# Kernel optimization log

Hardware: AMD Instinct MI355X
Metric: run time of the kernel (lower is better)

## Reference

```python
import jax, jax.numpy as jnp
import numpy as np

FILTER_SIZE = 27           # filter_size (K + 2)
K = FILTER_SIZE - 2        # sampled neighbors per central node
FEAT = 512                 # feature_dim
HID = 512                  # hidden_dim
NUM_NODES = 100000         # node-id universe for the features() embedding
B = 20000                  # batch of central nodes
ALPHA = 0.2                # leaky relu slope


def _star_eigvec(fs):
    # eigenvectors of I - D A D for the star graph on `fs` nodes (node 0 = hub)
    A = np.zeros((fs, fs))
    A[0, 1:] = 1.0
    A[1:, 0] = 1.0
    D = np.eye(fs)
    D[0, 0] = (fs - 1) ** (-0.5)
    L = np.eye(fs) - D @ A @ D
    _, u = np.linalg.eigh(L)
    return u.astype(np.float32)


def setup_inputs() -> dict:
    key = jax.random.key(0)
    k1, k2, k3, k4, k5 = jax.random.split(key, 5)
    nodes = jax.random.randint(k1, (B,), 0, NUM_NODES)
    neigh = jax.random.randint(k2, (B, K), 0, NUM_NODES)
    feat_table = jax.random.normal(k3, (NUM_NODES, FEAT), dtype=jnp.float32)
    # xavier_uniform for W [FEAT, HID] and a [2*HID]
    limW = float(np.sqrt(6.0 / (FEAT + HID)))
    W = jax.random.uniform(k4, (FEAT, HID), minval=-limW, maxval=limW, dtype=jnp.float32)
    lima = float(np.sqrt(6.0 / (1 + 2 * HID)))
    a_vec = jax.random.uniform(k5, (2 * HID,), minval=-lima, maxval=lima, dtype=jnp.float32)
    U = jnp.asarray(_star_eigvec(FILTER_SIZE))
    return {"nodes": nodes, "neigh": neigh, "feat_table": feat_table,
            "W": W, "a_vec": a_vec, "U": U}


def reference(nodes, neigh, feat_table, W, a_vec, U):
    # project features: input2 (central), input1 (neighbors)
    h_ct = feat_table[nodes] @ W                              # [B, H]
    h_nb = jnp.einsum('bkf,fh->bkh', feat_table[neigh], W)    # [B, K, H]
    # GAT-style edge scores: a @ [h_ct ; h_nb]
    s_ct = h_ct @ a_vec[:HID]                                 # [B]
    s_nb = h_nb @ a_vec[HID:]                                 # [B, K]
    logits = s_ct[:, None] + s_nb                             # [B, K]
    lrelu = jnp.where(logits > 0, logits, ALPHA * logits)
    edge_e = jnp.exp(-lrelu)                                  # [B, K]
    # per-row normalization (equals dense a1 rowsum: neighbors per row distinct)
    attn = edge_e / jnp.sum(edge_e, axis=1, keepdims=True)    # [B, K]
    # mask1: slots 1..K of each filter_size block hold attn * h_nb
    mask = attn[..., None] * h_nb                             # [B, K, H]
    m = jnp.pad(mask, ((0, 0), (1, 1), (0, 0)))               # [B, FILTER_SIZE, H]
    mt = jnp.swapaxes(m, 1, 2)                                # [B, H, FILTER_SIZE]
    # spectral transform: (mt @ U @ U^T) @ ones[FILTER_SIZE,1]
    avg = jnp.ones((FILTER_SIZE, 1), dtype=m.dtype)
    temp = ((mt @ U) @ U.T) @ avg                             # [B, H, 1]
    out = jnp.squeeze(temp, axis=-1)                          # [B, H]
    return jax.nn.relu(out)
```

## Files before the change

kernel.cpp:

```cpp
#include <hip/hip_runtime.h>
#include <stdint.h>
#include <string.h>

#define FEAT 512
#define HID 512
#define KNB 25
#define FS 27
#define NNODES 100000
#define ALPHA 0.2f

typedef short bf16x8 __attribute__((ext_vector_type(8)));
typedef float f32x4 __attribute__((ext_vector_type(4)));

__device__ __forceinline__ float bf2f(unsigned short u) {
    union { unsigned int i; float f; } x; x.i = ((unsigned int)u) << 16; return x.f;
}
__device__ __forceinline__ unsigned short f2bf(float f) {
    unsigned int x = __float_as_uint(f);
    unsigned int r = (x + 0x7fffu + ((x >> 16) & 1u)) >> 16;
    return (unsigned short)r;
}
__device__ __forceinline__ float ldf(const void* base, size_t idx, bool isf32) {
    return isf32 ? ((const float*)base)[idx] : bf2f(((const unsigned short*)base)[idx]);
}
__device__ __forceinline__ void gload16(const void* g, void* lds) {
    __builtin_amdgcn_global_load_lds(
        (const __attribute__((address_space(1))) unsigned int*)g,
        (__attribute__((address_space(3))) unsigned int*)lds, 16, 0, 0);
}

__global__ void detect_dtype(const void* __restrict__ feat, int* __restrict__ flag) {
    __shared__ int cnt;
    if (threadIdx.x == 0) cnt = 0;
    __syncthreads();
    const unsigned short* u = (const unsigned short*)feat;
    int c = 0;
    for (int i = threadIdx.x; i < 2048; i += 256) {
        float av = fabsf(bf2f(u[i]));
        if (!(av < 1e4f)) c++;
    }
    atomicAdd(&cnt, c);
    __syncthreads();
    if (threadIdx.x == 0) *flag = (cnt > 16) ? 1 : 0;
}

__global__ void prep_pq(const void* __restrict__ W, const void* __restrict__ a_vec,
                        const int* __restrict__ flag,
                        float* __restrict__ p, float* __restrict__ q) {
    bool isf32 = (*flag != 0);
    int f = blockIdx.x;
    int lane = threadIdx.x;
    float accp = 0.f, accq = 0.f;
    #pragma unroll
    for (int j = 0; j < 8; ++j) {
        int h = lane * 8 + j;
        float wv = ldf(W, (size_t)f * HID + h, isf32);
        accq += wv * ldf(a_vec, h, isf32);
        accp += wv * ldf(a_vec, HID + h, isf32);
    }
    #pragma unroll
    for (int off = 32; off > 0; off >>= 1) {
        accp += __shfl_down(accp, off);
        accq += __shfl_down(accq, off);
    }
    if (lane == 0) { p[f] = accp; q[f] = accq; }
}

__global__ void prep_M(const void* __restrict__ U, const int* __restrict__ flag,
                       float* __restrict__ Mv) {
    __shared__ float cs[FS];
    bool isf32 = (*flag != 0);
    int t = threadIdx.x;
    if (t < FS) {
        float c = 0.f;
        for (int i = 0; i < FS; ++i) c += ldf(U, i * FS + t, isf32);
        cs[t] = c;
    }
    __syncthreads();
    if (t < FS) {
        float m = 0.f;
        for (int j = 0; j < FS; ++j) m += ldf(U, t * FS + j, isf32) * cs[j];
        Mv[t] = m;
    }
}

__global__ void transposeW(const void* __restrict__ W, const int* __restrict__ flag,
                           unsigned short* __restrict__ Wt) {
    bool isf32 = (*flag != 0);
    int idx = blockIdx.x * blockDim.x + threadIdx.x;
    int n = idx >> 9, k = idx & (HID - 1);
    Wt[idx] = f2bf(ldf(W, (size_t)k * HID + n, isf32));
}

__global__ __launch_bounds__(256) void convert_score(
    const void* __restrict__ feat, const float* __restrict__ p,
    const float* __restrict__ q, const int* __restrict__ flag,
    unsigned short* __restrict__ featbf, float* __restrict__ sp,
    float* __restrict__ sq, int nRows) {
    bool isf32 = (*flag != 0);
    int wave = threadIdx.x >> 6, lane = threadIdx.x & 63;
    int row = blockIdx.x * 4 + wave;
    if (row >= nRows) return;
    float vals[8];
    if (isf32) {
        const float4* src = (const float4*)((const float*)feat + (size_t)row * FEAT) + lane * 2;
        float4 v0 = src[0], v1 = src[1];
        vals[0] = v0.x; vals[1] = v0.y; vals[2] = v0.z; vals[3] = v0.w;
        vals[4] = v1.x; vals[5] = v1.y; vals[6] = v1.z; vals[7] = v1.w;
        unsigned short o[8];
        #pragma unroll
        for (int j = 0; j < 8; ++j) o[j] = f2bf(vals[j]);
        *(uint4*)(&featbf[(size_t)row * FEAT + lane * 8]) = *(const uint4*)o;
    } else {
        uint4 v = *((const uint4*)((const unsigned short*)feat + (size_t)row * FEAT) + lane);
        unsigned int w4[4] = {v.x, v.y, v.z, v.w};
        #pragma unroll
        for (int j = 0; j < 4; ++j) {
            vals[2 * j]     = __uint_as_float(w4[j] << 16);
            vals[2 * j + 1] = __uint_as_float(w4[j] & 0xffff0000u);
        }
    }
    float accp = 0.f, accq = 0.f;
    const float* pv = p + lane * 8;
    const float* qv = q + lane * 8;
    #pragma unroll
    for (int j = 0; j < 8; ++j) { accp += vals[j] * pv[j]; accq += vals[j] * qv[j]; }
    #pragma unroll
    for (int off = 32; off > 0; off >>= 1) {
        accp += __shfl_down(accp, off);
        accq += __shfl_down(accq, off);
    }
    if (lane == 0) { sp[row] = accp; sq[row] = accq; }
}

__global__ __launch_bounds__(256) void attn_gather2(
    const void* __restrict__ feat, const unsigned short* __restrict__ featbf,
    const int* __restrict__ nodes, const int* __restrict__ neigh,
    const float* __restrict__ sp, const float* __restrict__ sq,
    const float* __restrict__ Mv, const int* __restrict__ flag,
    unsigned short* __restrict__ g, int B) {
    bool isf32 = (*flag != 0);
    const unsigned short* F = isf32 ? featbf : (const unsigned short*)feat;
    int wave = threadIdx.x >> 6, lane = threadIdx.x & 63;
    int b = blockIdx.x * 4 + wave;
    if (b >= B) return;
    int id = 0; float e = 0.f;
    if (lane < KNB) {
        id = neigh[(size_t)b * KNB + lane];
        float l = sq[nodes[b]] + sp[id];
        float lr = l > 0.f ? l : ALPHA * l;
        e = __expf(-lr);
    }
    float Z = e;
    #pragma unroll
    for (int off = 16; off > 0; off >>= 1) Z += __shfl_down(Z, off);
    Z = __shfl(Z, 0);
    float w = (lane < KNB) ? e * (1.f / Z) * Mv[lane + 1] : 0.f;
    float acc[8] = {0.f, 0.f, 0.f, 0.f, 0.f, 0.f, 0.f, 0.f};
    #pragma unroll
    for (int k = 0; k < KNB; ++k) {
        int idk = __builtin_amdgcn_readlane(id, k);
        float wk = __uint_as_float((unsigned int)__builtin_amdgcn_readlane(__float_as_int(w), k));
        uint4 v = *((const uint4*)(F + (size_t)idk * FEAT) + lane);
        unsigned int w4[4] = {v.x, v.y, v.z, v.w};
        #pragma unroll
        for (int j = 0; j < 4; ++j) {
            acc[2 * j]     += wk * __uint_as_float(w4[j] << 16);
            acc[2 * j + 1] += wk * __uint_as_float(w4[j] & 0xffff0000u);
        }
    }
    unsigned short o[8];
    #pragma unroll
    for (int j = 0; j < 8; ++j) o[j] = f2bf(acc[j]);
    *(uint4*)(&g[(size_t)b * FEAT + lane * 8]) = *(const uint4*)o;
}

__global__ __launch_bounds__(256) void attn_gather(
    const void* __restrict__ feat, const int* __restrict__ nodes,
    const int* __restrict__ neigh, const float* __restrict__ p,
    const float* __restrict__ q, const float* __restrict__ Mv,
    const int* __restrict__ flag, unsigned short* __restrict__ g) {
    __shared__ __attribute__((aligned(16))) unsigned short ldsF[KNB * FEAT];
    __shared__ float ldsS[KNB + 1];
    bool isf32 = (*flag != 0);
    int b = blockIdx.x;
    int t = threadIdx.x;
    int wave = t >> 6, lane = t & 63;
    for (int r = wave; r < KNB + 1; r += 4) {
        int id = (r == 0) ? nodes[b] : neigh[(size_t)b * KNB + (r - 1)];
        float vals[8];
        if (isf32) {
            const float4* row = (const float4*)((const float*)feat + (size_t)id * FEAT) + lane * 2;
            float4 v0 = row[0], v1 = row[1];
            vals[0] = v0.x; vals[1] = v0.y; vals[2] = v0.z; vals[3] = v0.w;
            vals[4] = v1.x; vals[5] = v1.y; vals[6] = v1.z; vals[7] = v1.w;
        } else {
            uint4 v = *((const uint4*)((const unsigned short*)feat + (size_t)id * FEAT) + lane);
            unsigned int w4[4] = {v.x, v.y, v.z, v.w};
            #pragma unroll
            for (int j = 0; j < 4; ++j) {
                vals[2 * j]     = bf2f((unsigned short)(w4[j] & 0xffffu));
                vals[2 * j + 1] = bf2f((unsigned short)(w4[j] >> 16));
            }
        }
        if (r > 0) {
            unsigned short o[8];
            #pragma unroll
            for (int j = 0; j < 8; ++j) o[j] = f2bf(vals[j]);
            *(uint4*)(&ldsF[(r - 1) * FEAT + lane * 8]) = *(const uint4*)o;
        }
        const float* vec = ((r == 0) ? q : p) + lane * 8;
        float acc = 0.f;
        #pragma unroll
        for (int j = 0; j < 8; ++j) acc += vals[j] * vec[j];
        #pragma unroll
        for (int off = 32; off > 0; off >>= 1) acc += __shfl_down(acc, off);
        if (lane == 0) ldsS[r] = acc;
    }
    __syncthreads();
    float s0 = ldsS[0];
    float w[KNB];
    float Z = 0.f;
    #pragma unroll
    for (int k = 0; k < KNB; ++k) {
        float l = s0 + ldsS[k + 1];
        float lr = l > 0.f ? l : ALPHA * l;
        float e = __expf(-lr);
        w[k] = e;
        Z += e;
    }
    float inv = 1.f / Z;
    #pragma unroll
    for (int k = 0; k < KNB; ++k) w[k] *= inv * Mv[k + 1];
    float acc0 = 0.f, acc1 = 0.f;
    #pragma unroll
    for (int k = 0; k < KNB; ++k) {
        unsigned int v = *(const unsigned int*)(&ldsF[k * FEAT + 2 * t]);
        acc0 += w[k] * bf2f((unsigned short)(v & 0xffffu));
        acc1 += w[k] * bf2f((unsigned short)(v >> 16));
    }
    unsigned int o = ((unsigned int)f2bf(acc1) << 16) | (unsigned int)f2bf(acc0);
    *(unsigned int*)(&g[(size_t)b * FEAT + 2 * t]) = o;
}

__global__ __launch_bounds__(256) void gemm_relu128(
    const unsigned short* __restrict__ G, const unsigned short* __restrict__ Wt,
    const int* __restrict__ flag, void* __restrict__ out, int M) {
    __shared__ __attribute__((aligned(16))) unsigned short As[128 * 64];
    __shared__ __attribute__((aligned(16))) unsigned short Bs[128 * 64];
    bool isf32 = (*flag != 0);
    int t = threadIdx.x;
    int wave = t >> 6, lane = t & 63;
    int mBase = blockIdx.y * 128;
    int nBase = blockIdx.x * 128;
    int wr = wave >> 1, wc = wave & 1;
    int fr = lane & 15, quad = lane >> 4;
    f32x4 acc[4][4];
    #pragma unroll
    for (int m = 0; m < 4; ++m)
        #pragma unroll
        for (int n = 0; n < 4; ++n) acc[m][n] = (f32x4){0.f, 0.f, 0.f, 0.f};

    int lrow = lane >> 3;
    int lcol = (lane & 7) * 8;
    for (int k0 = 0; k0 < FEAT; k0 += 64) {
        #pragma unroll
        for (int i = 0; i < 4; ++i) {
            int r = wave * 32 + i * 8;
            gload16(G + (size_t)(mBase + r + lrow) * FEAT + k0 + lcol, &As[r * 64]);
            gload16(Wt + (size_t)(nBase + r + lrow) * FEAT + k0 + lcol, &Bs[r * 64]);
        }
        __syncthreads();
        #pragma unroll
        for (int kk = 0; kk < 64; kk += 32) {
            bf16x8 av[4], bv[4];
            #pragma unroll
            for (int m = 0; m < 4; ++m)
                av[m] = *(const bf16x8*)(&As[(wr * 64 + m * 16 + fr) * 64 + kk + quad * 8]);
            #pragma unroll
            for (int n = 0; n < 4; ++n)
                bv[n] = *(const bf16x8*)(&Bs[(wc * 64 + n * 16 + fr) * 64 + kk + quad * 8]);
            #pragma unroll
            for (int m = 0; m < 4; ++m)
                #pragma unroll
                for (int n = 0; n < 4; ++n)
                    acc[m][n] = __builtin_amdgcn_mfma_f32_16x16x32_bf16(av[m], bv[n], acc[m][n], 0, 0, 0);
        }
        __syncthreads();
    }
    int col = lane & 15, qr = (lane >> 4) * 4;
    #pragma unroll
    for (int m = 0; m < 4; ++m) {
        #pragma unroll
        for (int n = 0; n < 4; ++n) {
            #pragma unroll
            for (int i = 0; i < 4; ++i) {
                int row = mBase + wr * 64 + m * 16 + qr + i;
                if (row < M) {
                    int cn = nBase + wc * 64 + n * 16 + col;
                    float v = acc[m][n][i];
                    v = v > 0.f ? v : 0.f;
                    size_t off = (size_t)row * HID + cn;
                    if (isf32) ((float*)out)[off] = v;
                    else ((unsigned short*)out)[off] = f2bf(v);
                }
            }
        }
    }
}

__global__ __launch_bounds__(256) void gemm_relu(
    const unsigned short* __restrict__ G, const unsigned short* __restrict__ Wt,
    const int* __restrict__ flag, void* __restrict__ out, int M) {
    __shared__ __attribute__((aligned(16))) unsigned short As[64 * 72];
    __shared__ __attribute__((aligned(16))) unsigned short Bs[64 * 72];
    bool isf32 = (*flag != 0);
    int t = threadIdx.x;
    int mBase = blockIdx.y * 64;
    int nBase = blockIdx.x * 64;
    int wave = t >> 6, lane = t & 63;
    int mOff = (wave & 1) * 32, nOff = (wave >> 1) * 32;
    f32x4 acc00 = {0.f, 0.f, 0.f, 0.f}, acc01 = {0.f, 0.f, 0.f, 0.f};
    f32x4 acc10 = {0.f, 0.f, 0.f, 0.f}, acc11 = {0.f, 0.f, 0.f, 0.f};
    int lr = t >> 2;
    int seg = (t & 3) * 16;
    int fr = lane & 15, quad = lane >> 4;
    for (int k0 = 0; k0 < FEAT; k0 += 64) {
        uint4 av0 = {0u, 0u, 0u, 0u}, av1 = {0u, 0u, 0u, 0u};
        int gr = mBase + lr;
        if (gr < M) {
            const unsigned short* s = G + (size_t)gr * FEAT + k0 + seg;
            av0 = *(const uint4*)s;
            av1 = *(const uint4*)(s + 8);
        }
        *(uint4*)(&As[lr * 72 + seg]) = av0;
        *(uint4*)(&As[lr * 72 + seg + 8]) = av1;
        const unsigned short* bs = Wt + (size_t)(nBase + lr) * FEAT + k0 + seg;
        *(uint4*)(&Bs[lr * 72 + seg]) = *(const uint4*)bs;
        *(uint4*)(&Bs[lr * 72 + seg + 8]) = *(const uint4*)(bs + 8);
        __syncthreads();
        #pragma unroll
        for (int kk = 0; kk < 64; kk += 32) {
            bf16x8 a0 = *(const bf16x8*)(&As[(mOff + fr) * 72 + kk + quad * 8]);
            bf16x8 a1 = *(const bf16x8*)(&As[(mOff + 16 + fr) * 72 + kk + quad * 8]);
            bf16x8 b0 = *(const bf16x8*)(&Bs[(nOff + fr) * 72 + kk + quad * 8]);
            bf16x8 b1 = *(const bf16x8*)(&Bs[(nOff + 16 + fr) * 72 + kk + quad * 8]);
            acc00 = __builtin_amdgcn_mfma_f32_16x16x32_bf16(a0, b0, acc00, 0, 0, 0);
            acc01 = __builtin_amdgcn_mfma_f32_16x16x32_bf16(a0, b1, acc01, 0, 0, 0);
            acc10 = __builtin_amdgcn_mfma_f32_16x16x32_bf16(a1, b0, acc10, 0, 0, 0);
            acc11 = __builtin_amdgcn_mfma_f32_16x16x32_bf16(a1, b1, acc11, 0, 0, 0);
        }
        __syncthreads();
    }
    int col = lane & 15, qr = (lane >> 4) * 4;
    #pragma unroll
    for (int sel = 0; sel < 4; ++sel) {
        f32x4 a = (sel == 0) ? acc00 : (sel == 1) ? acc01 : (sel == 2) ? acc10 : acc11;
        int mt = sel >> 1, nt = sel & 1;
        #pragma unroll
        for (int i = 0; i < 4; ++i) {
            int row = mBase + mOff + mt * 16 + qr + i;
            if (row < M) {
                int cn = nBase + nOff + nt * 16 + col;
                float v = a[i];
                v = v > 0.f ? v : 0.f;
                size_t off = (size_t)row * HID + cn;
                if (isf32) ((float*)out)[off] = v;
                else ((unsigned short*)out)[off] = f2bf(v);
            }
        }
    }
}

extern "C" void kernel_launch(void* const* d_in, const int* in_sizes, int n_in,
                              void* d_out, int out_size, void* d_ws, size_t ws_size,
                              hipStream_t stream) {
    const int* nodes = (const int*)d_in[0];
    const int* neigh = (const int*)d_in[1];
    const void* feat = d_in[2];
    const void* W = d_in[3];
    const void* a_vec = d_in[4];
    const void* U = d_in[5];
    int B = in_sizes[0];

    char* ws = (char*)d_ws;
    int* flag = (int*)ws;
    float* p = (float*)(ws + 256);
    float* q = (float*)(ws + 256 + 2048);
    float* Mv = (float*)(ws + 256 + 4096);
    unsigned short* Wt = (unsigned short*)(ws + 4608);
    unsigned short* g = (unsigned short*)(ws + 4608 + (size_t)FEAT * HID * 2);
    size_t gEnd = 4608 + (size_t)FEAT * HID * 2 + (size_t)B * FEAT * 2;
    float* sp = (float*)(ws + gEnd);
    float* sq = (float*)(ws + gEnd + (size_t)NNODES * 4);
    unsigned short* featbf = (unsigned short*)(ws + gEnd + (size_t)NNODES * 8);
    size_t need = gEnd + (size_t)NNODES * 8 + (size_t)NNODES * FEAT * 2;

    detect_dtype<<<1, 256, 0, stream>>>(feat, flag);
    prep_pq<<<FEAT, 64, 0, stream>>>(W, a_vec, flag, p, q);
    prep_M<<<1, 32, 0, stream>>>(U, flag, Mv);
    transposeW<<<(FEAT * HID) / 256, 256, 0, stream>>>(W, flag, Wt);
    if (ws_size >= need) {
        convert_score<<<(NNODES + 3) / 4, 256, 0, stream>>>(feat, p, q, flag, featbf, sp, sq, NNODES);
        attn_gather2<<<(B + 3) / 4, 256, 0, stream>>>(feat, featbf, nodes, neigh, sp, sq, Mv, flag, g, B);
        dim3 gg(HID / 128, (B + 127) / 128);
        gemm_relu128<<<gg, 256, 0, stream>>>(g, Wt, flag, d_out, B);
    } else {
        attn_gather<<<B, 256, 0, stream>>>(feat, nodes, neigh, p, q, Mv, flag, g);
        dim3 gg(HID / 64, (B + 63) / 64);
        gemm_relu<<<gg, 256, 0, stream>>>(g, Wt, flag, d_out, B);
    }
}
```

Baseline: 428.2 us.

## Project all node features first, then gather projected rows with fused ReLU

The feature-to-bf16 conversion, neighbor gather and final GEMM are replaced by two kernels. The first is a GEMM projecting the whole node table by W that also computes the per-node attention scores in the same pass. The second gathers the projected bf16 rows with attention weights and writes the ReLU output directly. This drops the separate conversion pass, the intermediate aggregated buffer and the batch GEMM, and relies on aggregation commuting with the linear projection. The cost is projecting every table node instead of only the batch (about five times more matrix FLOPs) and re-reading fp32 features once per column block.

```diff
diff --git a/kernel.cpp b/kernel.cpp
--- a/kernel.cpp
+++ b/kernel.cpp
@@ -92,55 +92,120 @@
     Wt[idx] = f2bf(ldf(W, (size_t)k * HID + n, isf32));
 }
 
-__global__ __launch_bounds__(256) void convert_score(
-    const void* __restrict__ feat, const float* __restrict__ p,
-    const float* __restrict__ q, const int* __restrict__ flag,
-    unsigned short* __restrict__ featbf, float* __restrict__ sp,
-    float* __restrict__ sq, int nRows) {
-    bool isf32 = (*flag != 0);
-    int wave = threadIdx.x >> 6, lane = threadIdx.x & 63;
-    int row = blockIdx.x * 4 + wave;
-    if (row >= nRows) return;
-    float vals[8];
-    if (isf32) {
-        const float4* src = (const float4*)((const float*)feat + (size_t)row * FEAT) + lane * 2;
-        float4 v0 = src[0], v1 = src[1];
-        vals[0] = v0.x; vals[1] = v0.y; vals[2] = v0.z; vals[3] = v0.w;
-        vals[4] = v1.x; vals[5] = v1.y; vals[6] = v1.z; vals[7] = v1.w;
-        unsigned short o[8];
-        #pragma unroll
-        for (int j = 0; j < 8; ++j) o[j] = f2bf(vals[j]);
-        *(uint4*)(&featbf[(size_t)row * FEAT + lane * 8]) = *(const uint4*)o;
-    } else {
-        uint4 v = *((const uint4*)((const unsigned short*)feat + (size_t)row * FEAT) + lane);
-        unsigned int w4[4] = {v.x, v.y, v.z, v.w};
-        #pragma unroll
-        for (int j = 0; j < 4; ++j) {
-            vals[2 * j]     = __uint_as_float(w4[j] << 16);
-            vals[2 * j + 1] = __uint_as_float(w4[j] & 0xffff0000u);
-        }
-    }
-    float accp = 0.f, accq = 0.f;
-    const float* pv = p + lane * 8;
-    const float* qv = q + lane * 8;
-    #pragma unroll
-    for (int j = 0; j < 8; ++j) { accp += vals[j] * pv[j]; accq += vals[j] * qv[j]; }
-    #pragma unroll
-    for (int off = 32; off > 0; off >>= 1) {
-        accp += __shfl_down(accp, off);
-        accq += __shfl_down(accq, off);
-    }
-    if (lane == 0) { sp[row] = accp; sq[row] = accq; }
-}
-
-__global__ __launch_bounds__(256) void attn_gather2(
-    const void* __restrict__ feat, const unsigned short* __restrict__ featbf,
-    const int* __restrict__ nodes, const int* __restrict__ neigh,
-    const float* __restrict__ sp, const float* __restrict__ sq,
-    const float* __restrict__ Mv, const int* __restrict__ flag,
-    unsigned short* __restrict__ g, int B) {
-    bool isf32 = (*flag != 0);
-    const unsigned short* F = isf32 ? featbf : (const unsigned short*)feat;
+__global__ __launch_bounds__(256) void hgemm_score(
+    const void* __restrict__ feat, const unsigned short* __restrict__ Wt,
+    const float* __restrict__ p, const float* __restrict__ q,
+    const int* __restrict__ flag, unsigned short* __restrict__ H,
+    float* __restrict__ sp, float* __restrict__ sq, int nRows) {
+    __shared__ __attribute__((aligned(16))) unsigned short As[128 * 72];
+    __shared__ __attribute__((aligned(16))) unsigned short Bs[128 * 64];
+    bool isf32 = (*flag != 0);
+    int t = threadIdx.x;
+    int wave = t >> 6, lane = t & 63;
+    int mBase = blockIdx.y * 128;
+    int nBase = blockIdx.x * 128;
+    bool doScore = (blockIdx.x == 0);
+    int wr = wave >> 1, wc = wave & 1;
+    int fr = lane & 15, quad = lane >> 4;
+    f32x4 acc[4][4];
+    #pragma unroll
+    for (int m = 0; m < 4; ++m)
+        #pragma unroll
+        for (int n = 0; n < 4; ++n) acc[m][n] = (f32x4){0.f, 0.f, 0.f, 0.f};
+    float accp[8], accq[8];
+    #pragma unroll
+    for (int j = 0; j < 8; ++j) { accp[j] = 0.f; accq[j] = 0.f; }
+
+    int lrow = lane >> 3;
+    int lcol = (lane & 7) * 8;
+    int rBase = t >> 4;
+    int kv = t & 15;
+
+    for (int k0 = 0; k0 < FEAT; k0 += 64) {
+        #pragma unroll
+        for (int i = 0; i < 4; ++i) {
+            int r = wave * 32 + i * 8;
+            gload16(Wt + (size_t)(nBase + r + lrow) * FEAT + k0 + lcol, &Bs[r * 64]);
+        }
+        float4 pv = {0.f, 0.f, 0.f, 0.f}, qv = {0.f, 0.f, 0.f, 0.f};
+        if (doScore) {
+            pv = *(const float4*)(p + k0 + kv * 4);
+            qv = *(const float4*)(q + k0 + kv * 4);
+        }
+        #pragma unroll
+        for (int j = 0; j < 8; ++j) {
+            int row = j * 16 + rBase;
+            int gr = mBase + row;
+            if (gr > nRows - 1) gr = nRows - 1;
+            float4 f;
+            if (isf32) {
+                f = *((const float4*)((const float*)feat + (size_t)gr * FEAT + k0) + kv);
+            } else {
+                ushort4 uv = *((const ushort4*)((const unsigned short*)feat + (size_t)gr * FEAT + k0) + kv);
+                f.x = bf2f(uv.x); f.y = bf2f(uv.y); f.z = bf2f(uv.z); f.w = bf2f(uv.w);
+            }
+            if (doScore) {
+                accp[j] += f.x * pv.x + f.y * pv.y + f.z * pv.z + f.w * pv.w;
+                accq[j] += f.x * qv.x + f.y * qv.y + f.z * qv.z + f.w * qv.w;
+            }
+            ushort4 o;
+            o.x = f2bf(f.x); o.y = f2bf(f.y); o.z = f2bf(f.z); o.w = f2bf(f.w);
+            *(ushort4*)(&As[row * 72 + kv * 4]) = o;
+        }
+        __syncthreads();
+        #pragma unroll
+        for (int kk = 0; kk < 64; kk += 32) {
+            bf16x8 av[4], bv[4];
+            #pragma unroll
+            for (int m = 0; m < 4; ++m)
+                av[m] = *(const bf16x8*)(&As[(wr * 64 + m * 16 + fr) * 72 + kk + quad * 8]);
+            #pragma unroll
+            for (int n = 0; n < 4; ++n)
+                bv[n] = *(const bf16x8*)(&Bs[(wc * 64 + n * 16 + fr) * 64 + kk + quad * 8]);
+            #pragma unroll
+            for (int m = 0; m < 4; ++m)
+                #pragma unroll
+                for (int n = 0; n < 4; ++n)
+                    acc[m][n] = __builtin_amdgcn_mfma_f32_16x16x32_bf16(av[m], bv[n], acc[m][n], 0, 0, 0);
+        }
+        __syncthreads();
+    }
+    if (doScore) {
+        #pragma unroll
+        for (int j = 0; j < 8; ++j) {
+            float ap = accp[j], aq = accq[j];
+            #pragma unroll
+            for (int off = 1; off < 16; off <<= 1) {
+                ap += __shfl_xor(ap, off);
+                aq += __shfl_xor(aq, off);
+            }
+            if (kv == 0) {
+                int row = mBase + j * 16 + rBase;
+                if (row < nRows) { sp[row] = ap; sq[row] = aq; }
+            }
+        }
+    }
+    int col = lane & 15, qr = (lane >> 4) * 4;
+    #pragma unroll
+    for (int m = 0; m < 4; ++m) {
+        #pragma unroll
+        for (int n = 0; n < 4; ++n) {
+            #pragma unroll
+            for (int i = 0; i < 4; ++i) {
+                int row = mBase + wr * 64 + m * 16 + qr + i;
+                int cn = nBase + wc * 64 + n * 16 + col;
+                H[(size_t)row * HID + cn] = f2bf(acc[m][n][i]);
+            }
+        }
+    }
+}
+
+__global__ __launch_bounds__(256) void gather_out(
+    const unsigned short* __restrict__ H, const int* __restrict__ nodes,
+    const int* __restrict__ neigh, const float* __restrict__ sp,
+    const float* __restrict__ sq, const float* __restrict__ Mv,
+    const int* __restrict__ flag, void* __restrict__ out, int B) {
+    bool isf32 = (*flag != 0);
     int wave = threadIdx.x >> 6, lane = threadIdx.x & 63;
     int b = blockIdx.x * 4 + wave;
     if (b >= B) return;
@@ -161,7 +226,7 @@
     for (int k = 0; k < KNB; ++k) {
         int idk = __builtin_amdgcn_readlane(id, k);
         float wk = __uint_as_float((unsigned int)__builtin_amdgcn_readlane(__float_as_int(w), k));
-        uint4 v = *((const uint4*)(F + (size_t)idk * FEAT) + lane);
+        uint4 v = *((const uint4*)(H + (size_t)idk * HID) + lane);
         unsigned int w4[4] = {v.x, v.y, v.z, v.w};
         #pragma unroll
         for (int j = 0; j < 4; ++j) {
@@ -169,10 +234,19 @@
             acc[2 * j + 1] += wk * __uint_as_float(w4[j] & 0xffff0000u);
         }
     }
-    unsigned short o[8];
-    #pragma unroll
-    for (int j = 0; j < 8; ++j) o[j] = f2bf(acc[j]);
-    *(uint4*)(&g[(size_t)b * FEAT + lane * 8]) = *(const uint4*)o;
+    #pragma unroll
+    for (int j = 0; j < 8; ++j) acc[j] = acc[j] > 0.f ? acc[j] : 0.f;
+    if (isf32) {
+        float4 o0 = {acc[0], acc[1], acc[2], acc[3]};
+        float4 o1 = {acc[4], acc[5], acc[6], acc[7]};
+        float4* dst = (float4*)((float*)out + (size_t)b * HID) + lane * 2;
+        dst[0] = o0; dst[1] = o1;
+    } else {
+        unsigned short o[8];
+        #pragma unroll
+        for (int j = 0; j < 8; ++j) o[j] = f2bf(acc[j]);
+        *(uint4*)((unsigned short*)out + (size_t)b * HID + lane * 8) = *(const uint4*)o;
+    }
 }
 
 __global__ __launch_bounds__(256) void attn_gather(
@@ -241,72 +315,6 @@
     }
     unsigned int o = ((unsigned int)f2bf(acc1) << 16) | (unsigned int)f2bf(acc0);
     *(unsigned int*)(&g[(size_t)b * FEAT + 2 * t]) = o;
-}
-
-__global__ __launch_bounds__(256) void gemm_relu128(
-    const unsigned short* __restrict__ G, const unsigned short* __restrict__ Wt,
-    const int* __restrict__ flag, void* __restrict__ out, int M) {
-    __shared__ __attribute__((aligned(16))) unsigned short As[128 * 64];
-    __shared__ __attribute__((aligned(16))) unsigned short Bs[128 * 64];
-    bool isf32 = (*flag != 0);
-    int t = threadIdx.x;
-    int wave = t >> 6, lane = t & 63;
-    int mBase = blockIdx.y * 128;
-    int nBase = blockIdx.x * 128;
-    int wr = wave >> 1, wc = wave & 1;
-    int fr = lane & 15, quad = lane >> 4;
-    f32x4 acc[4][4];
-    #pragma unroll
-    for (int m = 0; m < 4; ++m)
-        #pragma unroll
-        for (int n = 0; n < 4; ++n) acc[m][n] = (f32x4){0.f, 0.f, 0.f, 0.f};
-
-    int lrow = lane >> 3;
-    int lcol = (lane & 7) * 8;
-    for (int k0 = 0; k0 < FEAT; k0 += 64) {
-        #pragma unroll
-        for (int i = 0; i < 4; ++i) {
-            int r = wave * 32 + i * 8;
-            gload16(G + (size_t)(mBase + r + lrow) * FEAT + k0 + lcol, &As[r * 64]);
-            gload16(Wt + (size_t)(nBase + r + lrow) * FEAT + k0 + lcol, &Bs[r * 64]);
-        }
-        __syncthreads();
-        #pragma unroll
-        for (int kk = 0; kk < 64; kk += 32) {
-            bf16x8 av[4], bv[4];
-            #pragma unroll
-            for (int m = 0; m < 4; ++m)
-                av[m] = *(const bf16x8*)(&As[(wr * 64 + m * 16 + fr) * 64 + kk + quad * 8]);
-            #pragma unroll
-            for (int n = 0; n < 4; ++n)
-                bv[n] = *(const bf16x8*)(&Bs[(wc * 64 + n * 16 + fr) * 64 + kk + quad * 8]);
-            #pragma unroll
-            for (int m = 0; m < 4; ++m)
-                #pragma unroll
-                for (int n = 0; n < 4; ++n)
-                    acc[m][n] = __builtin_amdgcn_mfma_f32_16x16x32_bf16(av[m], bv[n], acc[m][n], 0, 0, 0);
-        }
-        __syncthreads();
-    }
-    int col = lane & 15, qr = (lane >> 4) * 4;
-    #pragma unroll
-    for (int m = 0; m < 4; ++m) {
-        #pragma unroll
-        for (int n = 0; n < 4; ++n) {
-            #pragma unroll
-            for (int i = 0; i < 4; ++i) {
-                int row = mBase + wr * 64 + m * 16 + qr + i;
-                if (row < M) {
-                    int cn = nBase + wc * 64 + n * 16 + col;
-                    float v = acc[m][n][i];
-                    v = v > 0.f ? v : 0.f;
-                    size_t off = (size_t)row * HID + cn;
-                    if (isf32) ((float*)out)[off] = v;
-                    else ((unsigned short*)out)[off] = f2bf(v);
-                }
-            }
-        }
-    }
 }
 
 __global__ __launch_bounds__(256) void gemm_relu(
@@ -389,23 +397,25 @@
     float* q = (float*)(ws + 256 + 2048);
     float* Mv = (float*)(ws + 256 + 4096);
     unsigned short* Wt = (unsigned short*)(ws + 4608);
-    unsigned short* g = (unsigned short*)(ws + 4608 + (size_t)FEAT * HID * 2);
-    size_t gEnd = 4608 + (size_t)FEAT * HID * 2 + (size_t)B * FEAT * 2;
-    float* sp = (float*)(ws + gEnd);
-    float* sq = (float*)(ws + gEnd + (size_t)NNODES * 4);
-    unsigned short* featbf = (unsigned short*)(ws + gEnd + (size_t)NNODES * 8);
-    size_t need = gEnd + (size_t)NNODES * 8 + (size_t)NNODES * FEAT * 2;
+    size_t spOff = 4608 + (size_t)FEAT * HID * 2;
+    float* sp = (float*)(ws + spOff);
+    float* sq = (float*)(ws + spOff + (size_t)NNODES * 4);
+    size_t hOff = spOff + (size_t)NNODES * 8;
+    hOff = (hOff + 255) & ~(size_t)255;
+    int hRows = ((NNODES + 127) / 128) * 128;
+    unsigned short* H = (unsigned short*)(ws + hOff);
+    size_t need = hOff + (size_t)hRows * HID * 2;
 
     detect_dtype<<<1, 256, 0, stream>>>(feat, flag);
     prep_pq<<<FEAT, 64, 0, stream>>>(W, a_vec, flag, p, q);
     prep_M<<<1, 32, 0, stream>>>(U, flag, Mv);
     transposeW<<<(FEAT * HID) / 256, 256, 0, stream>>>(W, flag, Wt);
     if (ws_size >= need) {
-        convert_score<<<(NNODES + 3) / 4, 256, 0, stream>>>(feat, p, q, flag, featbf, sp, sq, NNODES);
-        attn_gather2<<<(B + 3) / 4, 256, 0, stream>>>(feat, featbf, nodes, neigh, sp, sq, Mv, flag, g, B);
-        dim3 gg(HID / 128, (B + 127) / 128);
-        gemm_relu128<<<gg, 256, 0, stream>>>(g, Wt, flag, d_out, B);
+        dim3 gh(HID / 128, (NNODES + 127) / 128);
+        hgemm_score<<<gh, 256, 0, stream>>>(feat, Wt, p, q, flag, H, sp, sq, NNODES);
+        gather_out<<<(B + 3) / 4, 256, 0, stream>>>(H, nodes, neigh, sp, sq, Mv, flag, d_out, B);
     } else {
+        unsigned short* g = (unsigned short*)(ws + spOff);
         attn_gather<<<B, 256, 0, stream>>>(feat, nodes, neigh, p, q, Mv, flag, g);
         dim3 gg(HID / 64, (B + 63) / 64);
         gemm_relu<<<gg, 256, 0, stream>>>(g, Wt, flag, d_out, B);
```

New measurement: 645.9 us. 1.51x slower.
